# Kernel optimization log

Hardware: AMD Instinct MI355X
Metric: run time of the kernel (lower is better)

## Reference

```python
import jax, jax.numpy as jnp
import numpy as np

NUM_HEAD = 8
HEAD_DIM = 64
TEMPERATURE = 10000.0


def positional_encoding(L, D):
    # Mirrors get_positional_encoding: sin on even-indexed, cos on odd-indexed
    # columns of pos, interleaved via stack+reshape.
    embed = jnp.arange(L, dtype=jnp.float32)
    dim_t = jnp.arange(D, dtype=jnp.float32)
    dim_t = TEMPERATURE ** (2.0 * jnp.floor(dim_t / 2.0) / D)
    pos = embed[:, None] / dim_t                      # [L, D]
    pos = jnp.stack([jnp.sin(pos[:, 0::2]), jnp.cos(pos[:, 1::2])], axis=2)
    return pos.reshape(1, L, D)                       # [1, L, D]


def setup_inputs() -> dict:
    key = jax.random.key(0)
    ks = jax.random.split(key, 4)
    B, L, D = 8, 1024, 256
    HD = NUM_HEAD * HEAD_DIM                          # 512
    glorot = float(np.sqrt(2.0 / (D + HD)))
    return {
        "x": jax.random.normal(ks[0], (B, L, D), jnp.float32),
        "Wq": jax.random.normal(ks[1], (D, HD), jnp.float32) * glorot,
        "bq": jnp.zeros((NUM_HEAD,), jnp.float32),
        "Wk": jax.random.normal(ks[2], (D, HD), jnp.float32) * glorot,
        "bk": jnp.zeros((NUM_HEAD,), jnp.float32),
        "Wv": jax.random.normal(ks[3], (D, HD), jnp.float32) * glorot,
        "bv": jnp.zeros((NUM_HEAD,), jnp.float32),
    }


def reference(x, Wq, bq, Wk, bk, Wv, bv):
    B, L, D = x.shape
    pe = positional_encoding(L, D)
    qk_in = x + pe                                    # query/key get pos-enc, value does not
    # per-head bias broadcast over head_dim (tf.repeat(bias, head_dim))
    q = qk_in @ Wq + jnp.repeat(bq, HEAD_DIM)
    k = qk_in @ Wk + jnp.repeat(bk, HEAD_DIM)
    v = x @ Wv + jnp.repeat(bv, HEAD_DIM)
    split = lambda t: t.reshape(B, L, NUM_HEAD, HEAD_DIM)
    q, k, v = split(q), split(k), split(v)
    att = jnp.einsum('blhd,bmhd->bhlm', q, k) * (float(HEAD_DIM) ** -0.5)
    att = jax.nn.softmax(att, axis=-1)                # [B, H, L, L]
    out = jnp.einsum('bhlm,bmhd->blhd', att, v)       # [B, L, H, hd]
    return out.reshape(B, L, NUM_HEAD * HEAD_DIM)
```

## Files before the change

kernel.cpp:

```cpp
#include <hip/hip_runtime.h>
#include <hip/hip_bf16.h>

#define NB   8
#define NL   1024
#define ND   256
#define NH   8
#define NHD  64
#define NC   512
#define NTOK (NB*NL)

typedef __bf16 bf16x8v __attribute__((ext_vector_type(8)));
typedef float f32x4 __attribute__((ext_vector_type(4)));

__device__ __forceinline__ unsigned short f2bf(float f) {
  unsigned u = __float_as_uint(f);
  unsigned r = (u + 0x7fffu + ((u >> 16) & 1u)) >> 16;
  return (unsigned short)r;
}

__device__ __forceinline__ unsigned pack_bf16x2(float lo, float hi) {
  __hip_bfloat162 h2 = __float22bfloat162_rn(make_float2(lo, hi));
  union { __hip_bfloat162 h; unsigned u; } cvt;
  cvt.h = h2;
  return cvt.u;
}

__global__ __launch_bounds__(256) void prep_kernel(
    const float* __restrict__ x,
    const float* __restrict__ Wq, const float* __restrict__ Wk,
    const float* __restrict__ Wv,
    unsigned short* __restrict__ xpe, unsigned short* __restrict__ xb,
    unsigned short* __restrict__ wqt, unsigned short* __restrict__ wkt,
    unsigned short* __restrict__ wvt) {
  int bid = blockIdx.x;
  if (bid < (NTOK * ND) / 256) {
    int idx = bid * 256 + threadIdx.x;
    int d = idx & (ND - 1);
    int t = idx >> 8;
    int l = t & (NL - 1);
    float xv = x[idx];
    float inv_dim = __expf(-9.210340371976184f * (float)(d >> 1) * (1.0f / 128.0f));
    float ang = (float)l * inv_dim;
    float pe = (d & 1) ? cosf(ang) : sinf(ang);
    xpe[idx] = f2bf(xv + pe);
    xb[idx]  = f2bf(xv);
  } else {
    int idx = (bid - (NTOK * ND) / 256) * 256 + threadIdx.x;
    int m = idx >> 17;
    int r = idx & (NC * ND - 1);
    const float* W = (m == 0) ? Wq : (m == 1) ? Wk : Wv;
    unsigned short* Wt = (m == 0) ? wqt : (m == 1) ? wkt : wvt;
    int k = r & (ND - 1);
    int n = r >> 8;
    Wt[r] = f2bf(W[k * NC + n]);
  }
}

__global__ __launch_bounds__(256) void gemm_qkv_kernel(
    const unsigned short* __restrict__ xpe, const unsigned short* __restrict__ xb,
    const unsigned short* __restrict__ wqt, const unsigned short* __restrict__ wkt,
    const unsigned short* __restrict__ wvt,
    const float* __restrict__ bq, const float* __restrict__ bk,
    const float* __restrict__ bv,
    unsigned short* __restrict__ qg, unsigned short* __restrict__ kg,
    unsigned short* __restrict__ vg) {
  __shared__ unsigned short As[128 * 72];
  __shared__ unsigned short Bs[64 * 72];

  const int z = blockIdx.z;
  const unsigned short* X  = (z == 2) ? xb : xpe;
  const unsigned short* Wt = (z == 0) ? wqt : (z == 1) ? wkt : wvt;
  const float* bias        = (z == 0) ? bq  : (z == 1) ? bk  : bv;
  unsigned short* Out      = (z == 0) ? qg  : (z == 1) ? kg  : vg;
  const float scale        = (z == 0) ? 0.125f : 1.0f;

  const int nt = blockIdx.x;
  const int mt = blockIdx.y;
  const int tid = threadIdx.x;
  const int w = tid >> 6;
  const int lane = tid & 63;
  const int lg = lane >> 4;
  const int lr = lane & 15;

  f32x4 acc[2][4] = {};

  for (int kb = 0; kb < 4; ++kb) {
#pragma unroll
    for (int i = 0; i < 4; ++i) {
      int slot = tid + i * 256;
      int r = slot >> 3, c8 = slot & 7;
      *(int4*)(As + r * 72 + c8 * 8) =
          *(const int4*)(X + (mt * 128 + r) * ND + kb * 64 + c8 * 8);
    }
#pragma unroll
    for (int i = 0; i < 2; ++i) {
      int slot = tid + i * 256;
      int r = slot >> 3, c8 = slot & 7;
      *(int4*)(Bs + r * 72 + c8 * 8) =
          *(const int4*)(Wt + (nt * 64 + r) * ND + kb * 64 + c8 * 8);
    }
    __syncthreads();

#pragma unroll
    for (int kk = 0; kk < 2; ++kk) {
      bf16x8v a[2], b[4];
#pragma unroll
      for (int mi = 0; mi < 2; ++mi)
        a[mi] = *(const bf16x8v*)(As + (w * 32 + mi * 16 + lr) * 72 + kk * 32 + lg * 8);
#pragma unroll
      for (int nb = 0; nb < 4; ++nb)
        b[nb] = *(const bf16x8v*)(Bs + (nb * 16 + lr) * 72 + kk * 32 + lg * 8);
#pragma unroll
      for (int mi = 0; mi < 2; ++mi)
#pragma unroll
        for (int nb = 0; nb < 4; ++nb)
          acc[mi][nb] = __builtin_amdgcn_mfma_f32_16x16x32_bf16(
              a[mi], b[nb], acc[mi][nb], 0, 0, 0);
    }
    __syncthreads();
  }

#pragma unroll
  for (int mi = 0; mi < 2; ++mi) {
#pragma unroll
    for (int nb = 0; nb < 4; ++nb) {
#pragma unroll
      for (int j = 0; j < 4; ++j) {
        int r = mt * 128 + w * 32 + mi * 16 + lg * 4 + j;
        int c = nt * 64 + nb * 16 + lr;
        int bb = r >> 10, lpos = r & (NL - 1);
        int h = c >> 6, dd = c & 63;
        float val = (acc[mi][nb][j] + bias[h]) * scale;
        if (z < 2)
          Out[((bb * NH + h) * NL + lpos) * NHD + dd] = f2bf(val);
        else
          Out[((bb * NH + h) * NHD + dd) * NL + lpos] = f2bf(val);
      }
    }
  }
}

__global__ __launch_bounds__(256) void attn_kernel(
    const unsigned short* __restrict__ Q,
    const unsigned short* __restrict__ K,
    const unsigned short* __restrict__ Vt,
    float* __restrict__ Out) {
  __shared__ unsigned short Ks[64 * 72];
  __shared__ unsigned short Vs[64 * 72];
  __shared__ unsigned short Ps[64 * 72];

  const int qt = blockIdx.x;
  const int bh = blockIdx.y;
  const int bb = bh >> 3, h = bh & 7;
  const int tid = threadIdx.x;
  const int w = tid >> 6;
  const int lane = tid & 63;
  const int lg = lane >> 4, lr = lane & 15;
  const int qrow0 = qt * 64 + w * 16;

  bf16x8v qf[2];
#pragma unroll
  for (int kk = 0; kk < 2; ++kk)
    qf[kk] = *(const bf16x8v*)(Q + ((size_t)bh * NL + qrow0 + lr) * NHD + kk * 32 + lg * 8);

  float m_ = -1e30f, lsum = 0.0f;
  f32x4 o[4] = {};

  for (int kv = 0; kv < 16; ++kv) {
#pragma unroll
    for (int i = 0; i < 2; ++i) {
      int slot = tid + i * 256;
      int r = slot >> 3, c8 = slot & 7;
      *(int4*)(Ks + r * 72 + c8 * 8) =
          *(const int4*)(K + ((size_t)bh * NL + kv * 64 + r) * NHD + c8 * 8);
      *(int4*)(Vs + r * 72 + c8 * 8) =
          *(const int4*)(Vt + ((size_t)bh * NHD + r) * NL + kv * 64 + c8 * 8);
    }
    __syncthreads();

    f32x4 s[4] = {};
#pragma unroll
    for (int kk = 0; kk < 2; ++kk) {
#pragma unroll
      for (int nb = 0; nb < 4; ++nb) {
        bf16x8v kf = *(const bf16x8v*)(Ks + (nb * 16 + lr) * 72 + kk * 32 + lg * 8);
        s[nb] = __builtin_amdgcn_mfma_f32_16x16x32_bf16(kf, qf[kk], s[nb], 0, 0, 0);
      }
    }

    float tm = s[0][0];
#pragma unroll
    for (int nb = 0; nb < 4; ++nb)
#pragma unroll
      for (int j = 0; j < 4; ++j) tm = fmaxf(tm, s[nb][j]);
    tm = fmaxf(tm, __shfl_xor(tm, 16, 64));
    tm = fmaxf(tm, __shfl_xor(tm, 32, 64));
    float nm = fmaxf(m_, tm);
    float corr = __expf(m_ - nm);
    m_ = nm;
    float ts = 0.0f;
#pragma unroll
    for (int nb = 0; nb < 4; ++nb)
#pragma unroll
      for (int j = 0; j < 4; ++j) {
        float p = __expf(s[nb][j] - nm);
        s[nb][j] = p;
        ts += p;
      }
    ts += __shfl_xor(ts, 16, 64);
    ts += __shfl_xor(ts, 32, 64);
    lsum = lsum * corr + ts;
#pragma unroll
    for (int db = 0; db < 4; ++db)
#pragma unroll
      for (int j = 0; j < 4; ++j) o[db][j] *= corr;

#pragma unroll
    for (int nb = 0; nb < 4; ++nb)
#pragma unroll
      for (int hh = 0; hh < 2; ++hh)
        *(unsigned*)(Ps + (w * 16 + lr) * 72 + nb * 16 + lg * 4 + 2 * hh) =
            pack_bf16x2(s[nb][2 * hh], s[nb][2 * hh + 1]);

#pragma unroll
    for (int kk = 0; kk < 2; ++kk) {
      bf16x8v pf = *(const bf16x8v*)(Ps + (w * 16 + lr) * 72 + kk * 32 + lg * 8);
#pragma unroll
      for (int db = 0; db < 4; ++db) {
        bf16x8v vf = *(const bf16x8v*)(Vs + (db * 16 + lr) * 72 + kk * 32 + lg * 8);
        o[db] = __builtin_amdgcn_mfma_f32_16x16x32_bf16(vf, pf, o[db], 0, 0, 0);
      }
    }
    __syncthreads();
  }

  float inv = 1.0f / lsum;
  int q = qrow0 + lr;
#pragma unroll
  for (int db = 0; db < 4; ++db) {
    f32x4 ov;
#pragma unroll
    for (int j = 0; j < 4; ++j) ov[j] = o[db][j] * inv;
    *(f32x4*)(Out + (size_t)(bb * NL + q) * NC + h * NHD + db * 16 + lg * 4) = ov;
  }
}

extern "C" void kernel_launch(void* const* d_in, const int* in_sizes, int n_in,
                              void* d_out, int out_size, void* d_ws, size_t ws_size,
                              hipStream_t stream) {
  const float* x  = (const float*)d_in[0];
  const float* Wq = (const float*)d_in[1];
  const float* bq = (const float*)d_in[2];
  const float* Wk = (const float*)d_in[3];
  const float* bk = (const float*)d_in[4];
  const float* Wv = (const float*)d_in[5];
  const float* bv = (const float*)d_in[6];
  float* out = (float*)d_out;

  unsigned short* xpe = (unsigned short*)d_ws;
  unsigned short* xb  = xpe + (size_t)NTOK * ND;
  unsigned short* wqt = xb  + (size_t)NTOK * ND;
  unsigned short* wkt = wqt + (size_t)ND * NC;
  unsigned short* wvt = wkt + (size_t)ND * NC;
  unsigned short* qg  = wvt + (size_t)ND * NC;
  unsigned short* kg  = qg  + (size_t)NB * NH * NL * NHD;
  unsigned short* vg  = kg  + (size_t)NB * NH * NL * NHD;

  int prep_blocks = (NTOK * ND) / 256 + 3 * (NC * ND) / 256;
  prep_kernel<<<prep_blocks, 256, 0, stream>>>(x, Wq, Wk, Wv, xpe, xb, wqt, wkt, wvt);

  gemm_qkv_kernel<<<dim3(8, 64, 3), 256, 0, stream>>>(
      xpe, xb, wqt, wkt, wvt, bq, bk, bv, qg, kg, vg);

  attn_kernel<<<dim3(16, 64), 256, 0, stream>>>(qg, kg, vg, out);
}
```

Before: 155.0 us.

## Vectorize prep, tile weight transpose, prefetch tiles, use exp2 softmax with lazy rescale

The prep kernel now handles eight elements per thread with vector loads and stores and fast sin/cos, and transposes the weights through a shared-memory tile so global accesses coalesce. The QKV GEMM and attention kernels load the next tile into registers while computing on the current one, which removes one barrier per iteration. The softmax folds log2(e) into the Q scale, switches to exp2, and rescales the running max and accumulator only when some lane's max grows by more than 8. Fast trig and the skipped rescale change numerics slightly, and the prefetch buffers raise register pressure.

```diff
diff --git a/kernel.cpp b/kernel.cpp
--- a/kernel.cpp
+++ b/kernel.cpp
@@ -32,27 +32,52 @@
     unsigned short* __restrict__ xpe, unsigned short* __restrict__ xb,
     unsigned short* __restrict__ wqt, unsigned short* __restrict__ wkt,
     unsigned short* __restrict__ wvt) {
-  int bid = blockIdx.x;
-  if (bid < (NTOK * ND) / 256) {
-    int idx = bid * 256 + threadIdx.x;
-    int d = idx & (ND - 1);
-    int t = idx >> 8;
+  const int bid = blockIdx.x;
+  const int tid = threadIdx.x;
+  if (bid < (NTOK * ND) / (256 * 8)) {
+    int idx = bid * 256 + tid;
+    int d0 = (idx & 31) * 8;
+    int t = idx >> 5;
     int l = t & (NL - 1);
-    float xv = x[idx];
-    float inv_dim = __expf(-9.210340371976184f * (float)(d >> 1) * (1.0f / 128.0f));
-    float ang = (float)l * inv_dim;
-    float pe = (d & 1) ? cosf(ang) : sinf(ang);
-    xpe[idx] = f2bf(xv + pe);
-    xb[idx]  = f2bf(xv);
+    float4 xa = *(const float4*)(x + (size_t)t * ND + d0);
+    float4 xc = *(const float4*)(x + (size_t)t * ND + d0 + 4);
+    float xv[8] = {xa.x, xa.y, xa.z, xa.w, xc.x, xc.y, xc.z, xc.w};
+    unsigned short pe_out[8], xb_out[8];
+#pragma unroll
+    for (int p = 0; p < 4; ++p) {
+      float inv_dim = __expf(-0.07195578415606394f * (float)(d0 / 2 + p));
+      float ang = (float)l * inv_dim;
+      float sv = __sinf(ang);
+      float cv = __cosf(ang);
+      pe_out[2 * p]     = f2bf(xv[2 * p] + sv);
+      pe_out[2 * p + 1] = f2bf(xv[2 * p + 1] + cv);
+      xb_out[2 * p]     = f2bf(xv[2 * p]);
+      xb_out[2 * p + 1] = f2bf(xv[2 * p + 1]);
+    }
+    *(int4*)(xpe + (size_t)t * ND + d0) = *(int4*)pe_out;
+    *(int4*)(xb  + (size_t)t * ND + d0) = *(int4*)xb_out;
   } else {
-    int idx = (bid - (NTOK * ND) / 256) * 256 + threadIdx.x;
-    int m = idx >> 17;
-    int r = idx & (NC * ND - 1);
+    __shared__ float tile[64 * 65];
+    int widx = bid - (NTOK * ND) / (256 * 8);
+    int m = widx >> 5;
+    int tl = widx & 31;
+    int kt = tl & 3;
+    int nt = tl >> 2;
     const float* W = (m == 0) ? Wq : (m == 1) ? Wk : Wv;
     unsigned short* Wt = (m == 0) ? wqt : (m == 1) ? wkt : wvt;
-    int k = r & (ND - 1);
-    int n = r >> 8;
-    Wt[r] = f2bf(W[k * NC + n]);
+    int c = tid & 63, rb = tid >> 6;
+#pragma unroll
+    for (int i = 0; i < 16; ++i) {
+      int r = i * 4 + rb;
+      tile[r * 65 + c] = W[(kt * 64 + r) * NC + nt * 64 + c];
+    }
+    __syncthreads();
+#pragma unroll
+    for (int i = 0; i < 16; ++i) {
+      int n_local = i * 4 + rb, k_local = c;
+      Wt[(nt * 64 + n_local) * ND + kt * 64 + k_local] =
+          f2bf(tile[k_local * 65 + n_local]);
+    }
   }
 }
 
@@ -72,7 +97,7 @@
   const unsigned short* Wt = (z == 0) ? wqt : (z == 1) ? wkt : wvt;
   const float* bias        = (z == 0) ? bq  : (z == 1) ? bk  : bv;
   unsigned short* Out      = (z == 0) ? qg  : (z == 1) ? kg  : vg;
-  const float scale        = (z == 0) ? 0.125f : 1.0f;
+  const float scale        = (z == 0) ? 0.18033688011112042f : 1.0f;
 
   const int nt = blockIdx.x;
   const int mt = blockIdx.y;
@@ -83,22 +108,40 @@
   const int lr = lane & 15;
 
   f32x4 acc[2][4] = {};
-
+  int4 areg[4], breg[2];
+
+  auto load_tiles = [&](int kb) {
+#pragma unroll
+    for (int i = 0; i < 4; ++i) {
+      int slot = tid + i * 256;
+      int r = slot >> 3, c8 = slot & 7;
+      areg[i] = *(const int4*)(X + (mt * 128 + r) * ND + kb * 64 + c8 * 8);
+    }
+#pragma unroll
+    for (int i = 0; i < 2; ++i) {
+      int slot = tid + i * 256;
+      int r = slot >> 3, c8 = slot & 7;
+      breg[i] = *(const int4*)(Wt + (nt * 64 + r) * ND + kb * 64 + c8 * 8);
+    }
+  };
+
+  load_tiles(0);
+#pragma unroll
   for (int kb = 0; kb < 4; ++kb) {
+    if (kb) __syncthreads();
 #pragma unroll
     for (int i = 0; i < 4; ++i) {
       int slot = tid + i * 256;
       int r = slot >> 3, c8 = slot & 7;
-      *(int4*)(As + r * 72 + c8 * 8) =
-          *(const int4*)(X + (mt * 128 + r) * ND + kb * 64 + c8 * 8);
+      *(int4*)(As + r * 72 + c8 * 8) = areg[i];
     }
 #pragma unroll
     for (int i = 0; i < 2; ++i) {
       int slot = tid + i * 256;
       int r = slot >> 3, c8 = slot & 7;
-      *(int4*)(Bs + r * 72 + c8 * 8) =
-          *(const int4*)(Wt + (nt * 64 + r) * ND + kb * 64 + c8 * 8);
-    }
+      *(int4*)(Bs + r * 72 + c8 * 8) = breg[i];
+    }
+    if (kb < 3) load_tiles(kb + 1);
     __syncthreads();
 
 #pragma unroll
@@ -117,7 +160,6 @@
           acc[mi][nb] = __builtin_amdgcn_mfma_f32_16x16x32_bf16(
               a[mi], b[nb], acc[mi][nb], 0, 0, 0);
     }
-    __syncthreads();
   }
 
 #pragma unroll
@@ -166,16 +208,28 @@
   float m_ = -1e30f, lsum = 0.0f;
   f32x4 o[4] = {};
 
+  int4 kreg[2], vreg[2];
+  auto load_kv = [&](int kv) {
+#pragma unroll
+    for (int i = 0; i < 2; ++i) {
+      int slot = tid + i * 256;
+      int r = slot >> 3, c8 = slot & 7;
+      kreg[i] = *(const int4*)(K + ((size_t)bh * NL + kv * 64 + r) * NHD + c8 * 8);
+      vreg[i] = *(const int4*)(Vt + ((size_t)bh * NHD + r) * NL + kv * 64 + c8 * 8);
+    }
+  };
+
+  load_kv(0);
   for (int kv = 0; kv < 16; ++kv) {
+    if (kv) __syncthreads();
 #pragma unroll
     for (int i = 0; i < 2; ++i) {
       int slot = tid + i * 256;
       int r = slot >> 3, c8 = slot & 7;
-      *(int4*)(Ks + r * 72 + c8 * 8) =
-          *(const int4*)(K + ((size_t)bh * NL + kv * 64 + r) * NHD + c8 * 8);
-      *(int4*)(Vs + r * 72 + c8 * 8) =
-          *(const int4*)(Vt + ((size_t)bh * NHD + r) * NL + kv * 64 + c8 * 8);
-    }
+      *(int4*)(Ks + r * 72 + c8 * 8) = kreg[i];
+      *(int4*)(Vs + r * 72 + c8 * 8) = vreg[i];
+    }
+    if (kv < 15) load_kv(kv + 1);
     __syncthreads();
 
     f32x4 s[4] = {};
@@ -195,25 +249,28 @@
       for (int j = 0; j < 4; ++j) tm = fmaxf(tm, s[nb][j]);
     tm = fmaxf(tm, __shfl_xor(tm, 16, 64));
     tm = fmaxf(tm, __shfl_xor(tm, 32, 64));
-    float nm = fmaxf(m_, tm);
-    float corr = __expf(m_ - nm);
-    m_ = nm;
+    if (__any(tm > m_ + 8.0f)) {
+      float nm = fmaxf(m_, tm);
+      float corr = exp2f(m_ - nm);
+      m_ = nm;
+      lsum *= corr;
+#pragma unroll
+      for (int db = 0; db < 4; ++db)
+#pragma unroll
+        for (int j = 0; j < 4; ++j) o[db][j] *= corr;
+    }
     float ts = 0.0f;
 #pragma unroll
     for (int nb = 0; nb < 4; ++nb)
 #pragma unroll
       for (int j = 0; j < 4; ++j) {
-        float p = __expf(s[nb][j] - nm);
+        float p = exp2f(s[nb][j] - m_);
         s[nb][j] = p;
         ts += p;
       }
     ts += __shfl_xor(ts, 16, 64);
     ts += __shfl_xor(ts, 32, 64);
-    lsum = lsum * corr + ts;
-#pragma unroll
-    for (int db = 0; db < 4; ++db)
-#pragma unroll
-      for (int j = 0; j < 4; ++j) o[db][j] *= corr;
+    lsum += ts;
 
 #pragma unroll
     for (int nb = 0; nb < 4; ++nb)
@@ -231,7 +288,6 @@
         o[db] = __builtin_amdgcn_mfma_f32_16x16x32_bf16(vf, pf, o[db], 0, 0, 0);
       }
     }
-    __syncthreads();
   }
 
   float inv = 1.0f / lsum;
@@ -266,7 +322,7 @@
   unsigned short* kg  = qg  + (size_t)NB * NH * NL * NHD;
   unsigned short* vg  = kg  + (size_t)NB * NH * NL * NHD;
 
-  int prep_blocks = (NTOK * ND) / 256 + 3 * (NC * ND) / 256;
+  int prep_blocks = (NTOK * ND) / (256 * 8) + 96;
   prep_kernel<<<prep_blocks, 256, 0, stream>>>(x, Wq, Wk, Wv, xpe, xb, wqt, wkt, wvt);
 
   gemm_qkv_kernel<<<dim3(8, 64, 3), 256, 0, stream>>>(
```

Measured after the change: 220.4 us. 1.42x slower.
